# Optimization experiments

Hardware: AMD Instinct MI355X
Metric: run time of the kernel (lower is better)

Reference implementation:

```python
import jax, jax.numpy as jnp
import numpy as np

B, D, M = 32, 640, 1024
EPS = 1e-05


def setup_inputs() -> dict:
    key = jax.random.key(0)
    x = jax.random.normal(key, (B, D, M), dtype=jnp.float32)
    return {"x": x}


def _triu_flat_indices(d):
    iu, ju = np.triu_indices(d)
    return jnp.asarray(iu * d + ju, dtype=jnp.int32)


def reference(x):
    b, d, m = x.shape
    # Gram matrix: x @ x^T  -> [b, d, d]
    x_pow2 = jnp.einsum('bim,bjm->bij', x, x)
    # I_M @ (x_pow2 * I) + (x_pow2 * I) @ I_M - 2*x_pow2
    # (x_pow2 * I) is diagonal, so ones-matrix bmm = broadcast of the diagonal.
    diag = jnp.diagonal(x_pow2, axis1=1, axis2=2)  # [b, d]
    dcov = diag[:, None, :] + diag[:, :, None] - 2.0 * x_pow2
    dcov = jnp.maximum(dcov, 0.0)
    # temperature param is built in-forward: exp(log(1/(2*d*m))) = 1/(2*d*m)
    temperature = 1.0 / (2.0 * d * m)
    dcov = jnp.sqrt(temperature * dcov + EPS)
    # Double centering: dcov @ I_M = row sums broadcast; I_M @ dcov = col sums.
    row_mean = dcov.sum(axis=2, keepdims=True) / d          # [b, d, 1]
    col_mean = dcov.sum(axis=1, keepdims=True) / d          # [b, 1, d]
    tot_mean = dcov.sum(axis=(1, 2), keepdims=True) / (d * d)
    t = dcov - row_mean - col_mean + tot_mean               # [b, d, d]
    # Triuvec: gather upper-triangular entries (incl. diagonal)
    flat_idx = _triu_flat_indices(d)                         # [d*(d+1)//2]
    y = t.reshape(b, d * d)[:, flat_idx]
    return y
```

## Files before the change

### kernel.cpp

```cpp
#include <hip/hip_runtime.h>

#define D_DIM 640
#define M_DIM 1024
#define B_DIM 32
#define BK 32
#define OUT_ROW 205120

typedef __bf16 bf16x8 __attribute__((ext_vector_type(8)));
typedef float f32x4 __attribute__((ext_vector_type(4)));

__device__ __forceinline__ unsigned short f2bf(float f) {
    union { float f; unsigned int u; } c; c.f = f;
    unsigned int u = c.u;
    unsigned int r = (u + 0x7fffu + ((u >> 16) & 1u)) >> 16;
    return (unsigned short)r;
}

__device__ __forceinline__ float bf2f(unsigned short h) {
    union { unsigned int u; float f; } c; c.u = ((unsigned int)h) << 16;
    return c.f;
}

__device__ __forceinline__ void gload_lds16(const unsigned short* g, unsigned short* l) {
    __builtin_amdgcn_global_load_lds(
        (const __attribute__((address_space(1))) unsigned int*)g,
        (__attribute__((address_space(3))) unsigned int*)l,
        16, 0, 0);
}

__device__ __forceinline__ float block_reduce_256(float s) {
    #pragma unroll
    for (int off = 32; off > 0; off >>= 1) s += __shfl_down(s, off, 64);
    __shared__ float red[4];
    if ((threadIdx.x & 63) == 0) red[threadIdx.x >> 6] = s;
    __syncthreads();
    return red[0] + red[1] + red[2] + red[3];
}

__global__ void cast_diag_kernel(const float* __restrict__ x,
                                 unsigned short* __restrict__ xb,
                                 float* __restrict__ diag,
                                 float* __restrict__ rowsum,
                                 float* __restrict__ tot) {
    const size_t row = blockIdx.x;
    const int t = threadIdx.x;
    const float4 v = ((const float4*)(x + row * M_DIM))[t];
    float s = v.x * v.x + v.y * v.y + v.z * v.z + v.w * v.w;
    ushort4 o;
    o.x = f2bf(v.x); o.y = f2bf(v.y); o.z = f2bf(v.z); o.w = f2bf(v.w);
    ((ushort4*)(xb + row * M_DIM))[t] = o;
    float ssum = block_reduce_256(s);
    if (t == 0) { diag[row] = ssum; rowsum[row] = 0.f; }
    if (t == 1 && row < B_DIM) tot[row] = 0.f;
}

__global__ __launch_bounds__(256, 2)
void gemm_dcov_kernel(const unsigned short* __restrict__ xb,
                      const float* __restrict__ diag,
                      unsigned short* __restrict__ dcov,
                      float* __restrict__ rowsum,
                      float* __restrict__ tot) {
    __shared__ __align__(16) unsigned short smem[32768];

    const int id = blockIdx.x;
    const int bt = (id & 7) * 4 + ((id >> 3) & 3);
    int p = id >> 5;
    int it = 0, off = p;
    while (off >= 5 - it) { off -= 5 - it; ++it; }
    const int jt = it + off;
    const bool diagTile = (it == jt);

    const int tid = threadIdx.x;
    const int w = tid >> 6, l = tid & 63;
    const int wy = w >> 1, wx = w & 1;
    const int lm = l & 15, quad = l >> 4;

    const unsigned short* gA = xb + ((size_t)bt * D_DIM + it * 128) * M_DIM;
    const unsigned short* gB = xb + ((size_t)bt * D_DIM + jt * 128) * M_DIM;

    const int r0 = tid >> 2;
    const int cl = (((tid & 3) ^ ((tid >> 3) & 3)) << 3);
    const size_t aoff1 = (size_t)r0 * M_DIM + cl;
    const size_t aoff2 = aoff1 + (size_t)64 * M_DIM;
    const int ldst = tid * 8;

    auto issue = [&](int k, int ph) {
        unsigned short* sA = smem + ph * 8192;
        unsigned short* sB = sA + 4096;
        const int koff = k * BK;
        gload_lds16(gA + aoff1 + koff, sA + ldst);
        gload_lds16(gA + aoff2 + koff, sA + ldst + 2048);
        gload_lds16(gB + aoff1 + koff, sB + ldst);
        gload_lds16(gB + aoff2 + koff, sB + ldst + 2048);
    };

    f32x4 acc[4][4];
    const f32x4 zero = {0.f, 0.f, 0.f, 0.f};
    #pragma unroll
    for (int i = 0; i < 4; i++)
        #pragma unroll
        for (int j = 0; j < 4; j++) acc[i][j] = zero;

    const int sw = ((quad ^ ((lm >> 1) & 3)) << 3);

    issue(0, 0); issue(1, 1); issue(2, 2);

    int ph = 0;
    for (int k = 0; k < 32; ++k) {
        if (k < 30)       asm volatile("s_waitcnt vmcnt(8)" ::: "memory");
        else if (k == 30) asm volatile("s_waitcnt vmcnt(4)" ::: "memory");
        else              asm volatile("s_waitcnt vmcnt(0)" ::: "memory");
        asm volatile("s_barrier" ::: "memory");
        if (k + 3 < 32) issue(k + 3, (ph + 3) & 3);

        const unsigned short* sA = smem + ph * 8192;
        const unsigned short* sB = sA + 4096;
        bf16x8 af[4], bfr[4];
        #pragma unroll
        for (int mi = 0; mi < 4; mi++)
            af[mi] = *(const bf16x8*)&sA[(wy * 64 + mi * 16 + lm) * BK + sw];
        #pragma unroll
        for (int ni = 0; ni < 4; ni++)
            bfr[ni] = *(const bf16x8*)&sB[(wx * 64 + ni * 16 + lm) * BK + sw];

        #pragma unroll
        for (int mi = 0; mi < 4; mi++)
            #pragma unroll
            for (int ni = 0; ni < 4; ni++)
                acc[mi][ni] = __builtin_amdgcn_mfma_f32_16x16x32_bf16(
                    af[mi], bfr[ni], acc[mi][ni], 0, 0, 0);

        ph = (ph + 1) & 3;
    }

    float* sd = (float*)smem;
    if (tid < 128) sd[tid] = diag[(size_t)bt * D_DIM + it * 128 + tid];
    else           sd[tid] = diag[(size_t)bt * D_DIM + jt * 128 + (tid - 128)];
    __syncthreads();

    const float temp = 7.62939453125e-07f;
    unsigned short* dbase = dcov + (size_t)bt * D_DIM * D_DIM;
    float* rs = rowsum + (size_t)bt * D_DIM;
    float ts = 0.f;
    float cp[4] = {0.f, 0.f, 0.f, 0.f};

    #pragma unroll
    for (int mi = 0; mi < 4; mi++) {
        #pragma unroll
        for (int r = 0; r < 4; r++) {
            const int lrow = wy * 64 + mi * 16 + quad * 4 + r;
            const int grow = it * 128 + lrow;
            const float di = sd[lrow];
            float rp = 0.f;
            #pragma unroll
            for (int ni = 0; ni < 4; ni++) {
                const int lcol = wx * 64 + ni * 16 + lm;
                const int gcol = jt * 128 + lcol;
                const float dj = sd[128 + lcol];
                const float g = acc[mi][ni][r];
                const float v = sqrtf(fmaf(temp, fmaxf(di + dj - 2.f * g, 0.f), 1e-5f));
                dbase[(size_t)grow * D_DIM + gcol] = f2bf(v);
                rp += v;
                cp[ni] += v;
            }
            ts += rp;
            rp += __shfl_down(rp, 8, 16);
            rp += __shfl_down(rp, 4, 16);
            rp += __shfl_down(rp, 2, 16);
            rp += __shfl_down(rp, 1, 16);
            if (lm == 0) atomicAdd(&rs[grow], rp);
        }
    }
    if (!diagTile) {
        #pragma unroll
        for (int ni = 0; ni < 4; ni++) {
            float c = cp[ni];
            c += __shfl_down(c, 32);
            c += __shfl_down(c, 16);
            if (l < 16) atomicAdd(&rs[jt * 128 + wx * 64 + ni * 16 + lm], c);
        }
    }
    float bs = block_reduce_256(ts);
    if (tid == 0) atomicAdd(&tot[bt], diagTile ? bs : 2.f * bs);
}

__global__ void output_kernel(const unsigned short* __restrict__ dcov,
                              const float* __restrict__ rowsum,
                              const float* __restrict__ tot,
                              float* __restrict__ out) {
    const int b = blockIdx.x / D_DIM;
    const int i = blockIdx.x - b * D_DIM;
    const float inv_d = 1.f / (float)D_DIM;
    const float rmi = rowsum[(size_t)b * D_DIM + i] * inv_d;
    const float tm = tot[b] * (inv_d * inv_d);
    const unsigned short* drow = dcov + ((size_t)b * D_DIM + i) * D_DIM;
    const float* rs = rowsum + (size_t)b * D_DIM;
    float* orow = out + (size_t)b * OUT_ROW + (size_t)i * D_DIM - (size_t)i * (i - 1) / 2;
    for (int j = i + threadIdx.x; j < D_DIM; j += 256)
        orow[j - i] = bf2f(drow[j]) - rmi - rs[j] * inv_d + tm;
}

extern "C" void kernel_launch(void* const* d_in, const int* in_sizes, int n_in,
                              void* d_out, int out_size, void* d_ws, size_t ws_size,
                              hipStream_t stream) {
    const float* x = (const float*)d_in[0];
    float* out = (float*)d_out;

    char* ws = (char*)d_ws;
    unsigned short* xb = (unsigned short*)ws;
    size_t off = 41943040;
    float* diag = (float*)(ws + off);           off += 81920;
    unsigned short* dcov = (unsigned short*)(ws + off); off += 26214400;
    float* rowsum = (float*)(ws + off);         off += 81920;
    float* tot = (float*)(ws + off);            off += 256;

    cast_diag_kernel<<<dim3(B_DIM * D_DIM), 256, 0, stream>>>(x, xb, diag, rowsum, tot);
    gemm_dcov_kernel<<<dim3(480), 256, 0, stream>>>(xb, diag, dcov, rowsum, tot);
    output_kernel<<<dim3(B_DIM * D_DIM), 256, 0, stream>>>(dcov, rowsum, tot, out);
}
```

Before: 171.5 us.

## Use single-wave 64x64 GEMM tiles and pair triangular rows in output kernel

Replaces the 4-wave 128x128 Gram tiles with single-wave 64x64 tiles, going from 15 to 55 triangular tiles per batch and 1760 blocks, with a 2-stage LDS double buffer and no block barriers. Diagonal values are read directly from global memory instead of staged through shared memory. The output kernel now handles row i and row 639-i in one block to balance the triangular work. This aims for better CU occupancy and load balance, at the cost of more redundant global loads per FLOP and a shallower prefetch pipeline.

```diff
diff --git a/kernel.cpp b/kernel.cpp
--- a/kernel.cpp
+++ b/kernel.cpp
@@ -3,7 +3,6 @@
 #define D_DIM 640
 #define M_DIM 1024
 #define B_DIM 32
-#define BK 32
 #define OUT_ROW 205120
 
 typedef __bf16 bf16x8 __attribute__((ext_vector_type(8)));
@@ -54,44 +53,41 @@
     if (t == 1 && row < B_DIM) tot[row] = 0.f;
 }
 
-__global__ __launch_bounds__(256, 2)
+__global__ __launch_bounds__(64, 2)
 void gemm_dcov_kernel(const unsigned short* __restrict__ xb,
                       const float* __restrict__ diag,
                       unsigned short* __restrict__ dcov,
                       float* __restrict__ rowsum,
                       float* __restrict__ tot) {
-    __shared__ __align__(16) unsigned short smem[32768];
+    __shared__ __align__(16) unsigned short smem[8192];
 
     const int id = blockIdx.x;
     const int bt = (id & 7) * 4 + ((id >> 3) & 3);
     int p = id >> 5;
     int it = 0, off = p;
-    while (off >= 5 - it) { off -= 5 - it; ++it; }
+    while (off >= 10 - it) { off -= 10 - it; ++it; }
     const int jt = it + off;
     const bool diagTile = (it == jt);
 
-    const int tid = threadIdx.x;
-    const int w = tid >> 6, l = tid & 63;
-    const int wy = w >> 1, wx = w & 1;
+    const int l = threadIdx.x;
     const int lm = l & 15, quad = l >> 4;
 
-    const unsigned short* gA = xb + ((size_t)bt * D_DIM + it * 128) * M_DIM;
-    const unsigned short* gB = xb + ((size_t)bt * D_DIM + jt * 128) * M_DIM;
-
-    const int r0 = tid >> 2;
-    const int cl = (((tid & 3) ^ ((tid >> 3) & 3)) << 3);
-    const size_t aoff1 = (size_t)r0 * M_DIM + cl;
-    const size_t aoff2 = aoff1 + (size_t)64 * M_DIM;
-    const int ldst = tid * 8;
+    const unsigned short* gA = xb + ((size_t)bt * D_DIM + it * 64) * M_DIM;
+    const unsigned short* gB = xb + ((size_t)bt * D_DIM + jt * 64) * M_DIM;
+
+    const int cl = (((l & 3) ^ ((l >> 3) & 3)) << 3);
+    const size_t goff = (size_t)(l >> 2) * M_DIM + cl;
+    const int ldst = l * 8;
 
     auto issue = [&](int k, int ph) {
-        unsigned short* sA = smem + ph * 8192;
-        unsigned short* sB = sA + 4096;
-        const int koff = k * BK;
-        gload_lds16(gA + aoff1 + koff, sA + ldst);
-        gload_lds16(gA + aoff2 + koff, sA + ldst + 2048);
-        gload_lds16(gB + aoff1 + koff, sB + ldst);
-        gload_lds16(gB + aoff2 + koff, sB + ldst + 2048);
+        unsigned short* sA = smem + ph * 4096;
+        unsigned short* sB = sA + 2048;
+        const int koff = k * 32;
+        #pragma unroll
+        for (int g = 0; g < 4; g++) {
+            gload_lds16(gA + goff + (size_t)g * 16 * M_DIM + koff, sA + g * 512 + ldst);
+            gload_lds16(gB + goff + (size_t)g * 16 * M_DIM + koff, sB + g * 512 + ldst);
+        }
     };
 
     f32x4 acc[4][4];
@@ -103,25 +99,25 @@
 
     const int sw = ((quad ^ ((lm >> 1) & 3)) << 3);
 
-    issue(0, 0); issue(1, 1); issue(2, 2);
-
-    int ph = 0;
+    issue(0, 0);
     for (int k = 0; k < 32; ++k) {
-        if (k < 30)       asm volatile("s_waitcnt vmcnt(8)" ::: "memory");
-        else if (k == 30) asm volatile("s_waitcnt vmcnt(4)" ::: "memory");
-        else              asm volatile("s_waitcnt vmcnt(0)" ::: "memory");
-        asm volatile("s_barrier" ::: "memory");
-        if (k + 3 < 32) issue(k + 3, (ph + 3) & 3);
-
-        const unsigned short* sA = smem + ph * 8192;
-        const unsigned short* sB = sA + 4096;
+        if (k + 1 < 32) {
+            issue(k + 1, (k + 1) & 1);
+            asm volatile("s_waitcnt vmcnt(8)" ::: "memory");
+        } else {
+            asm volatile("s_waitcnt vmcnt(0)" ::: "memory");
+        }
+
+        const unsigned short* sA = smem + (k & 1) * 4096;
+        const unsigned short* sB = sA + 2048;
         bf16x8 af[4], bfr[4];
         #pragma unroll
         for (int mi = 0; mi < 4; mi++)
-            af[mi] = *(const bf16x8*)&sA[(wy * 64 + mi * 16 + lm) * BK + sw];
+            af[mi] = *(const bf16x8*)&sA[(mi * 16 + lm) * 32 + sw];
         #pragma unroll
         for (int ni = 0; ni < 4; ni++)
-            bfr[ni] = *(const bf16x8*)&sB[(wx * 64 + ni * 16 + lm) * BK + sw];
+            bfr[ni] = *(const bf16x8*)&sB[(ni * 16 + lm) * 32 + sw];
+        asm volatile("s_waitcnt lgkmcnt(0)" ::: "memory");
 
         #pragma unroll
         for (int mi = 0; mi < 4; mi++)
@@ -129,18 +125,17 @@
             for (int ni = 0; ni < 4; ni++)
                 acc[mi][ni] = __builtin_amdgcn_mfma_f32_16x16x32_bf16(
                     af[mi], bfr[ni], acc[mi][ni], 0, 0, 0);
-
-        ph = (ph + 1) & 3;
-    }
-
-    float* sd = (float*)smem;
-    if (tid < 128) sd[tid] = diag[(size_t)bt * D_DIM + it * 128 + tid];
-    else           sd[tid] = diag[(size_t)bt * D_DIM + jt * 128 + (tid - 128)];
-    __syncthreads();
+    }
 
     const float temp = 7.62939453125e-07f;
     unsigned short* dbase = dcov + (size_t)bt * D_DIM * D_DIM;
     float* rs = rowsum + (size_t)bt * D_DIM;
+    const float* dg = diag + (size_t)bt * D_DIM;
+
+    float dj[4];
+    #pragma unroll
+    for (int ni = 0; ni < 4; ni++) dj[ni] = dg[jt * 64 + ni * 16 + lm];
+
     float ts = 0.f;
     float cp[4] = {0.f, 0.f, 0.f, 0.f};
 
@@ -148,17 +143,15 @@
     for (int mi = 0; mi < 4; mi++) {
         #pragma unroll
         for (int r = 0; r < 4; r++) {
-            const int lrow = wy * 64 + mi * 16 + quad * 4 + r;
-            const int grow = it * 128 + lrow;
-            const float di = sd[lrow];
+            const int lrow = mi * 16 + quad * 4 + r;
+            const int grow = it * 64 + lrow;
+            const float di = dg[grow];
             float rp = 0.f;
             #pragma unroll
             for (int ni = 0; ni < 4; ni++) {
-                const int lcol = wx * 64 + ni * 16 + lm;
-                const int gcol = jt * 128 + lcol;
-                const float dj = sd[128 + lcol];
+                const int gcol = jt * 64 + ni * 16 + lm;
                 const float g = acc[mi][ni][r];
-                const float v = sqrtf(fmaf(temp, fmaxf(di + dj - 2.f * g, 0.f), 1e-5f));
+                const float v = sqrtf(fmaf(temp, fmaxf(di + dj[ni] - 2.f * g, 0.f), 1e-5f));
                 dbase[(size_t)grow * D_DIM + gcol] = f2bf(v);
                 rp += v;
                 cp[ni] += v;
@@ -177,27 +170,33 @@
             float c = cp[ni];
             c += __shfl_down(c, 32);
             c += __shfl_down(c, 16);
-            if (l < 16) atomicAdd(&rs[jt * 128 + wx * 64 + ni * 16 + lm], c);
-        }
-    }
-    float bs = block_reduce_256(ts);
-    if (tid == 0) atomicAdd(&tot[bt], diagTile ? bs : 2.f * bs);
+            if (l < 16) atomicAdd(&rs[jt * 64 + ni * 16 + lm], c);
+        }
+    }
+    #pragma unroll
+    for (int off = 32; off > 0; off >>= 1) ts += __shfl_down(ts, off, 64);
+    if (l == 0) atomicAdd(&tot[bt], diagTile ? ts : 2.f * ts);
 }
 
 __global__ void output_kernel(const unsigned short* __restrict__ dcov,
                               const float* __restrict__ rowsum,
                               const float* __restrict__ tot,
                               float* __restrict__ out) {
-    const int b = blockIdx.x / D_DIM;
-    const int i = blockIdx.x - b * D_DIM;
+    const int b = blockIdx.x / 320;
+    const int q = blockIdx.x - b * 320;
     const float inv_d = 1.f / (float)D_DIM;
-    const float rmi = rowsum[(size_t)b * D_DIM + i] * inv_d;
     const float tm = tot[b] * (inv_d * inv_d);
-    const unsigned short* drow = dcov + ((size_t)b * D_DIM + i) * D_DIM;
     const float* rs = rowsum + (size_t)b * D_DIM;
-    float* orow = out + (size_t)b * OUT_ROW + (size_t)i * D_DIM - (size_t)i * (i - 1) / 2;
-    for (int j = i + threadIdx.x; j < D_DIM; j += 256)
-        orow[j - i] = bf2f(drow[j]) - rmi - rs[j] * inv_d + tm;
+
+    #pragma unroll
+    for (int half = 0; half < 2; half++) {
+        const int i = half ? (D_DIM - 1 - q) : q;
+        const float rmi = rs[i] * inv_d;
+        const unsigned short* drow = dcov + ((size_t)b * D_DIM + i) * D_DIM;
+        float* orow = out + (size_t)b * OUT_ROW + (size_t)i * D_DIM - (size_t)i * (i - 1) / 2;
+        for (int j = i + threadIdx.x; j < D_DIM; j += 256)
+            orow[j - i] = bf2f(drow[j]) - rmi - rs[j] * inv_d + tm;
+    }
 }
 
 extern "C" void kernel_launch(void* const* d_in, const int* in_sizes, int n_in,
@@ -215,6 +214,6 @@
     float* tot = (float*)(ws + off);            off += 256;
 
     cast_diag_kernel<<<dim3(B_DIM * D_DIM), 256, 0, stream>>>(x, xb, diag, rowsum, tot);
-    gemm_dcov_kernel<<<dim3(480), 256, 0, stream>>>(xb, diag, dcov, rowsum, tot);
-    output_kernel<<<dim3(B_DIM * D_DIM), 256, 0, stream>>>(dcov, rowsum, tot, out);
-}
+    gemm_dcov_kernel<<<dim3(1760), 64, 0, stream>>>(xb, diag, dcov, rowsum, tot);
+    output_kernel<<<dim3(B_DIM * 320), 256, 0, stream>>>(dcov, rowsum, tot, out);
+}
```

Measured after the change: 184.8 us. 7.8% more time.
